# Performance work log

Hardware: AMD Instinct MI355X
Metric: run time of the kernel (lower is better)

The kernel has to match this reference:

```python
import jax, jax.numpy as jnp
import numpy as np

# ---- module hyperparameters (init_kwargs) ----
V0 = 1.0
SIGMA0 = 0.5
GAUSS_CONST = V0 / (np.sqrt(2.0 * np.pi) * SIGMA0)
NW, NF, D, H = 4096, 16, 3, 256  # walkers, fermions, dimensions, hidden width
N = NF * D


def setup_inputs() -> dict:
    key = jax.random.key(0)
    k0, k1, k2, k3 = jax.random.split(key, 4)
    sc = lambda k, shape, fan_in: jax.random.normal(k, shape, jnp.float32) / np.sqrt(fan_in).astype(np.float32)
    return {
        "x": jax.random.normal(k0, (NW, NF, D), jnp.float32),
        "W1": sc(k1, (N, H), N),
        "b1": jnp.zeros((H,), jnp.float32),
        "W2": sc(k2, (H, H), H),
        "b2": jnp.zeros((H,), jnp.float32),
        "w3": sc(k3, (H,), H),
        "b3": jnp.zeros((), jnp.float32),
    }


def _logpsi(xf, W1, b1, W2, b2, w3, b3):
    # xf: (N,) flattened single-walker coordinates -> scalar log|psi|
    h = jnp.tanh(xf @ W1 + b1)
    h = jnp.tanh(h @ W2 + b2)
    return h @ w3 + b3


def reference(x, W1, b1, W2, b2, w3, b3):
    nw, nf, d = x.shape
    xflat = x.reshape(nw, nf * d)

    f = lambda xf: _logpsi(xf, W1, b1, W2, b2, w3, b3)
    grad_f = jax.grad(f)

    def kinetic_one(xf):
        g = grad_f(xf)                      # (N,) d logpsi / dx
        hess = jax.jacfwd(grad_f)(xf)       # (N, N) forward-over-reverse Hessian
        lap = jnp.trace(hess)
        return -0.5 * (lap + jnp.sum(g * g))

    kin = jax.vmap(kinetic_one)(xflat)      # (nw,)

    # harmonic potential 1/2 sum x^2
    pot = 0.5 * jnp.sum(xflat * xflat, axis=1)

    # Gaussian interaction, faithful to source: unsqueeze(-2)/unsqueeze(-1) on
    # (nw, nf, d) broadcasts to (nw, nf, d, d) intra-particle coordinate diffs,
    # then sum over last axis -> (nw, nf, d), triu(k=1) over trailing (nf, d).
    diff = x[..., None, :] - x[..., :, None]            # (nw, nf, d, d)
    sqdist = jnp.sum(diff * diff, axis=-1)              # (nw, nf, d)
    mask = jnp.triu(jnp.ones((nf, d), x.dtype), k=1)    # (nf, d)
    inter = GAUSS_CONST * jnp.sum(jnp.exp(-sqdist / (2.0 * SIGMA0 ** 2)) * mask, axis=(-2, -1))

    eloc = kin + pot + inter
    return (eloc, kin, pot, inter)
```

## Files before the change

### kernel.cpp

```cpp
#include <hip/hip_runtime.h>
#include <cmath>

#define NWALK 4096
#define NXD   48
#define HID   256
#define WPB   8
#define GCONST 0.7978845608028654f

typedef _Float16 half8   __attribute__((ext_vector_type(8)));
typedef float    float4v __attribute__((ext_vector_type(4)));

__global__ __launch_bounds__(256) void prep_all(const float* __restrict__ W2,
                                                const float* __restrict__ W1,
                                                const float* __restrict__ x,
                                                const float* __restrict__ b1,
                                                _Float16* __restrict__ W2c,
                                                _Float16* __restrict__ W1c,
                                                _Float16* __restrict__ t1h,
                                                _Float16* __restrict__ h1h,
                                                _Float16* __restrict__ ch) {
    __shared__ float tile[64][65];
    __shared__ float xs[16][NXD];

    if (blockIdx.x < 16) {
        const int bi = blockIdx.x & 3;
        const int bj = blockIdx.x >> 2;
        const int tx = threadIdx.x & 63;
        const int ty = threadIdx.x >> 6;
        #pragma unroll
        for (int r = 0; r < 16; ++r) {
            int il = ty * 16 + r;
            tile[tx][il] = W2[(bi * 64 + il) * HID + bj * 64 + tx];
        }
        __syncthreads();
        #pragma unroll
        for (int r = 0; r < 16; ++r) {
            int jl = ty * 16 + r;
            W2c[(bj * 64 + jl) * HID + bi * 64 + tx] = (_Float16)tile[jl][tx];
        }
        #pragma unroll
        for (int r = 0; r < 3; ++r) {
            int k = blockIdx.x * 3 + r;
            W1c[k * HID + threadIdx.x] = (_Float16)W1[k * HID + threadIdx.x];
        }
    } else {
        const int i  = threadIdx.x;
        const int w0 = (blockIdx.x - 16) * 16;

        float col[NXD];
        float S = 0.f;
        #pragma unroll
        for (int k = 0; k < NXD; ++k) {
            float v = W1[k * HID + i];
            col[k] = v;
            S = fmaf(v, v, S);
        }
        #pragma unroll
        for (int t = threadIdx.x; t < 16 * NXD; t += 256)
            ((float*)xs)[t] = x[w0 * NXD + t];
        __syncthreads();

        const float b = b1[i];
        #pragma unroll 4
        for (int w = 0; w < 16; ++w) {
            float a1 = b;
            #pragma unroll
            for (int k = 0; k < NXD; ++k)
                a1 = fmaf(xs[w][k], col[k], a1);
            float h1 = tanhf(a1);
            float t1 = 1.f - h1 * h1;
            int off = (w0 + w) * HID + i;
            t1h[off] = (_Float16)t1;
            h1h[off] = (_Float16)h1;
            ch[off]  = (_Float16)(S * h1 * t1);
        }
    }
}

__global__ __launch_bounds__(256, 2) void eloc8(
    const float* __restrict__ x,
    const float* __restrict__ b2,
    const float* __restrict__ w3,
    const _Float16* __restrict__ W2c,
    const _Float16* __restrict__ W1c,
    const _Float16* __restrict__ t1h,
    const _Float16* __restrict__ h1h,
    const _Float16* __restrict__ ch,
    float* __restrict__ out)
{
    __shared__ __align__(16) _Float16 W1s[48 * HID];
    __shared__ float xs[WPB][NXD];
    __shared__ float gw[WPB][4][NXD];
    __shared__ float rt1p[WPB][4][16];
    __shared__ float us[WPB][HID], uhs[WPB][HID];
    __shared__ float b2s[HID], w3s[HID];
    __shared__ float r2s[4][WPB];
    __shared__ float rt2s[WPB];

    const int w0   = blockIdx.x * WPB;
    const int tid  = threadIdx.x;
    const int wave = tid >> 6;
    const int lane = tid & 63;
    const int n16  = lane & 15;
    const int quad = (tid >> 4) & 3;

    half8 afr[8][4];
    #pragma unroll
    for (int s = 0; s < 8; ++s)
        #pragma unroll
        for (int a = 0; a < 4; ++a)
            afr[s][a] = *(const half8*)(W2c + ((wave * 4 + a) * 16 + n16) * HID
                                        + s * 32 + quad * 8);

    b2s[tid] = b2[tid];
    w3s[tid] = w3[tid];
    #pragma unroll
    for (int t = tid; t < WPB * NXD; t += 256)
        ((float*)xs)[t] = x[w0 * NXD + t];

    #pragma unroll
    for (int t = tid; t < 48 * 32; t += 256) {
        int k = t >> 5, c = t & 31;
        half8 wv = *(const half8*)(W1c + k * HID + c * 8);
        *(half8*)(W1s + k * HID + ((c ^ (k & 7)) * 8)) = wv;
    }

    {
        const _Float16* src  = (n16 & 1) ? ch : h1h;
        const _Float16* brow = src + (size_t)(w0 + (n16 >> 1)) * HID;

        float4v acc[4];
        #pragma unroll
        for (int a = 0; a < 4; ++a) acc[a] = (float4v){0.f, 0.f, 0.f, 0.f};
        #pragma unroll
        for (int s = 0; s < 8; ++s) {
            half8 bf = *(const half8*)(brow + (s * 4 + quad) * 8);
            #pragma unroll
            for (int a = 0; a < 4; ++a)
                acc[a] = __builtin_amdgcn_mfma_f32_16x16x32_f16(afr[s][a], bf, acc[a], 0, 0, 0);
        }

        __syncthreads();

        const int w = n16 >> 1;
        float um[4][4];
        #pragma unroll
        for (int a = 0; a < 4; ++a)
            #pragma unroll
            for (int reg = 0; reg < 4; ++reg) um[a][reg] = 0.f;

        if (!(n16 & 1)) {
            #pragma unroll
            for (int a = 0; a < 4; ++a)
                #pragma unroll
                for (int reg = 0; reg < 4; ++reg) {
                    int i    = (wave * 4 + a) * 16 + quad * 4 + reg;
                    float a2 = acc[a][reg] + b2s[i];
                    float h2 = tanhf(a2);
                    float t2 = 1.f - h2 * h2;
                    float u  = w3s[i] * t2;
                    um[a][reg] = u;
                    us [w][i] = u;
                    uhs[w][i] = u * h2;
                }
        }

        float part = 0.f;
        #pragma unroll
        for (int a = 0; a < 4; ++a)
            #pragma unroll
            for (int reg = 0; reg < 4; ++reg) {
                float uo = __shfl_xor(um[a][reg], 1, 64);
                part = fmaf(uo, acc[a][reg], part);
            }
        part += __shfl_xor(part, 16, 64);
        part += __shfl_xor(part, 32, 64);
        if (quad == 0 && (n16 & 1)) r2s[wave][w] = part;
    }
    __syncthreads();
    if (tid < WPB)
        rt2s[tid] = r2s[0][tid] + r2s[1][tid] + r2s[2][tid] + r2s[3][tid];
    __syncthreads();

    #pragma unroll 1
    for (int ww = 0; ww < WPB; ++ww) {
        const int wg = w0 + ww;

        half8 t1f[8];
        #pragma unroll
        for (int s = 0; s < 8; ++s)
            t1f[s] = *(const half8*)(t1h + (size_t)wg * HID + (s * 4 + quad) * 8);

        float4v uu[4];
        #pragma unroll
        for (int a = 0; a < 4; ++a)
            uu[a] = *(const float4v*)(&us[ww][(wave * 4 + a) * 16 + quad * 4]);

        float4v sq[4];
        #pragma unroll
        for (int a = 0; a < 4; ++a) sq[a] = (float4v){0.f, 0.f, 0.f, 0.f};

        #pragma unroll 1
        for (int kt = 0; kt < 3; ++kt) {
            const int krow = kt * 16 + n16;

            half8 w1v[8];
            #pragma unroll
            for (int s = 0; s < 8; ++s)
                w1v[s] = *(const half8*)(W1s + krow * HID
                          + ((((s * 4 + quad) ^ (krow & 7)) << 3)));

            float4v acc[4];
            #pragma unroll
            for (int a = 0; a < 4; ++a) acc[a] = (float4v){0.f, 0.f, 0.f, 0.f};

            __builtin_amdgcn_s_setprio(1);
            #pragma unroll
            for (int s = 0; s < 8; ++s) {
                half8 bf = w1v[s] * t1f[s];
                #pragma unroll
                for (int a = 0; a < 4; ++a)
                    acc[a] = __builtin_amdgcn_mfma_f32_16x16x32_f16(
                        afr[s][a], bf, acc[a], 0, 0, 0);
            }
            __builtin_amdgcn_s_setprio(0);

            float g = 0.f;
            #pragma unroll
            for (int a = 0; a < 4; ++a)
                #pragma unroll
                for (int reg = 0; reg < 4; ++reg) {
                    float m = acc[a][reg];
                    sq[a][reg] = fmaf(m, m, sq[a][reg]);
                    g          = fmaf(m, uu[a][reg], g);
                }
            g += __shfl_xor(g, 16, 64);
            g += __shfl_xor(g, 32, 64);
            if (lane < 16) gw[ww][wave][kt * 16 + lane] = g;
        }

        float rt1 = 0.f;
        #pragma unroll
        for (int a = 0; a < 4; ++a) {
            float4v uh = *(const float4v*)(&uhs[ww][(wave * 4 + a) * 16 + quad * 4]);
            #pragma unroll
            for (int reg = 0; reg < 4; ++reg)
                rt1 = fmaf(sq[a][reg], uh[reg], rt1);
        }
        rt1 += __shfl_xor(rt1, 16, 64);
        rt1 += __shfl_xor(rt1, 32, 64);
        if (lane < 16) rt1p[ww][wave][lane] = rt1;
    }

    __syncthreads();

    const int wa = 2 * wave, wb = wa + 1;
    float rt2a = rt2s[wa];
    float rt2b = rt2s[wb];

    float r0 = rt1p[wa][quad][n16];
    float r1 = rt1p[wb][quad][n16];

    float ga = 0.f, gb = 0.f, xa = 0.f, xb = 0.f;
    if (lane < NXD) {
        ga = gw[wa][0][lane] + gw[wa][1][lane] + gw[wa][2][lane] + gw[wa][3][lane];
        gb = gw[wb][0][lane] + gw[wb][1][lane] + gw[wb][2][lane] + gw[wb][3][lane];
        xa = xs[wa][lane];
        xb = xs[wb][lane];
    }
    float gga = ga * ga, ggb = gb * gb;
    float pa = 0.5f * xa * xa, pb = 0.5f * xb * xb;
    #pragma unroll
    for (int off = 32; off > 0; off >>= 1) {
        r0  += __shfl_down(r0,  off, 64);
        r1  += __shfl_down(r1,  off, 64);
        gga += __shfl_down(gga, off, 64);
        ggb += __shfl_down(ggb, off, 64);
        pa  += __shfl_down(pa,  off, 64);
        pb  += __shfl_down(pb,  off, 64);
    }
    if (lane == 0) {
        float kina = r0 + rt2a - 0.5f * gga;
        float kinb = r1 + rt2b - 0.5f * ggb;

        float x0 = xs[wa][0], x1 = xs[wa][1], x2 = xs[wa][2];
        float x3 = xs[wa][3], x4 = xs[wa][4], x5 = xs[wa][5];
        float d01 = (x0-x1)*(x0-x1) + (x2-x1)*(x2-x1);
        float d02 = (x0-x2)*(x0-x2) + (x1-x2)*(x1-x2);
        float d12 = (x3-x5)*(x3-x5) + (x4-x5)*(x4-x5);
        float intera = GCONST * (expf(-2.f*d01) + expf(-2.f*d02) + expf(-2.f*d12));

        x0 = xs[wb][0]; x1 = xs[wb][1]; x2 = xs[wb][2];
        x3 = xs[wb][3]; x4 = xs[wb][4]; x5 = xs[wb][5];
        float e01 = (x0-x1)*(x0-x1) + (x2-x1)*(x2-x1);
        float e02 = (x0-x2)*(x0-x2) + (x1-x2)*(x1-x2);
        float e12 = (x3-x5)*(x3-x5) + (x4-x5)*(x4-x5);
        float interb = GCONST * (expf(-2.f*e01) + expf(-2.f*e02) + expf(-2.f*e12));

        const int wga = w0 + wa, wgb = w0 + wb;
        out[wga]             = kina + pa + intera;
        out[NWALK + wga]     = kina;
        out[2 * NWALK + wga] = pa;
        out[3 * NWALK + wga] = intera;
        out[wgb]             = kinb + pb + interb;
        out[NWALK + wgb]     = kinb;
        out[2 * NWALK + wgb] = pb;
        out[3 * NWALK + wgb] = interb;
    }
}

extern "C" void kernel_launch(void* const* d_in, const int* in_sizes, int n_in,
                              void* d_out, int out_size, void* d_ws, size_t ws_size,
                              hipStream_t stream) {
    const float* x  = (const float*)d_in[0];
    const float* W1 = (const float*)d_in[1];
    const float* b1 = (const float*)d_in[2];
    const float* W2 = (const float*)d_in[3];
    const float* b2 = (const float*)d_in[4];
    const float* w3 = (const float*)d_in[5];
    float* out = (float*)d_out;

    char* ws = (char*)d_ws;
    _Float16* W2c = (_Float16*)(ws);
    _Float16* W1c = (_Float16*)(ws + 131072);
    _Float16* t1h = (_Float16*)(ws + 155648);
    _Float16* h1h = (_Float16*)(ws + 2252800);
    _Float16* chv = (_Float16*)(ws + 4349952);

    prep_all<<<16 + NWALK / 16, 256, 0, stream>>>(W2, W1, x, b1, W2c, W1c, t1h, h1h, chv);
    eloc8<<<NWALK / WPB, 256, 0, stream>>>(x, b2, w3, W2c, W1c, t1h, h1h, chv, out);
}
```

Measured before the change: 110.3 us.

## Fuse prep kernel into main eloc kernel, computing layer-1 activations in shared memory

Removes the separate prep kernel. Each block now computes its own walkers' layer-1 tanh outputs (t1, h1, and the curvature term) into shared memory, converts W1 to fp16 in the block, and loads W2 transposed straight from fp32 global into MFMA fragments. This drops one kernel launch and the global round trip for the fp16 intermediates. In exchange every block repeats the weight conversion, reads W2 with a strided transposed pattern, and holds 48 W1 column values in registers, which raises register pressure and shared memory use.

```diff
diff --git a/kernel.cpp b/kernel.cpp
--- a/kernel.cpp
+++ b/kernel.cpp
@@ -10,89 +10,23 @@
 typedef _Float16 half8   __attribute__((ext_vector_type(8)));
 typedef float    float4v __attribute__((ext_vector_type(4)));
 
-__global__ __launch_bounds__(256) void prep_all(const float* __restrict__ W2,
-                                                const float* __restrict__ W1,
-                                                const float* __restrict__ x,
-                                                const float* __restrict__ b1,
-                                                _Float16* __restrict__ W2c,
-                                                _Float16* __restrict__ W1c,
-                                                _Float16* __restrict__ t1h,
-                                                _Float16* __restrict__ h1h,
-                                                _Float16* __restrict__ ch) {
-    __shared__ float tile[64][65];
-    __shared__ float xs[16][NXD];
-
-    if (blockIdx.x < 16) {
-        const int bi = blockIdx.x & 3;
-        const int bj = blockIdx.x >> 2;
-        const int tx = threadIdx.x & 63;
-        const int ty = threadIdx.x >> 6;
-        #pragma unroll
-        for (int r = 0; r < 16; ++r) {
-            int il = ty * 16 + r;
-            tile[tx][il] = W2[(bi * 64 + il) * HID + bj * 64 + tx];
-        }
-        __syncthreads();
-        #pragma unroll
-        for (int r = 0; r < 16; ++r) {
-            int jl = ty * 16 + r;
-            W2c[(bj * 64 + jl) * HID + bi * 64 + tx] = (_Float16)tile[jl][tx];
-        }
-        #pragma unroll
-        for (int r = 0; r < 3; ++r) {
-            int k = blockIdx.x * 3 + r;
-            W1c[k * HID + threadIdx.x] = (_Float16)W1[k * HID + threadIdx.x];
-        }
-    } else {
-        const int i  = threadIdx.x;
-        const int w0 = (blockIdx.x - 16) * 16;
-
-        float col[NXD];
-        float S = 0.f;
-        #pragma unroll
-        for (int k = 0; k < NXD; ++k) {
-            float v = W1[k * HID + i];
-            col[k] = v;
-            S = fmaf(v, v, S);
-        }
-        #pragma unroll
-        for (int t = threadIdx.x; t < 16 * NXD; t += 256)
-            ((float*)xs)[t] = x[w0 * NXD + t];
-        __syncthreads();
-
-        const float b = b1[i];
-        #pragma unroll 4
-        for (int w = 0; w < 16; ++w) {
-            float a1 = b;
-            #pragma unroll
-            for (int k = 0; k < NXD; ++k)
-                a1 = fmaf(xs[w][k], col[k], a1);
-            float h1 = tanhf(a1);
-            float t1 = 1.f - h1 * h1;
-            int off = (w0 + w) * HID + i;
-            t1h[off] = (_Float16)t1;
-            h1h[off] = (_Float16)h1;
-            ch[off]  = (_Float16)(S * h1 * t1);
-        }
-    }
-}
-
-__global__ __launch_bounds__(256, 2) void eloc8(
+__global__ __launch_bounds__(256, 2) void eloc_fused(
     const float* __restrict__ x,
+    const float* __restrict__ W1,
+    const float* __restrict__ b1,
+    const float* __restrict__ W2,
     const float* __restrict__ b2,
     const float* __restrict__ w3,
-    const _Float16* __restrict__ W2c,
-    const _Float16* __restrict__ W1c,
-    const _Float16* __restrict__ t1h,
-    const _Float16* __restrict__ h1h,
-    const _Float16* __restrict__ ch,
     float* __restrict__ out)
 {
     __shared__ __align__(16) _Float16 W1s[48 * HID];
+    __shared__ __align__(16) _Float16 t1s[WPB][HID];
+    __shared__ __align__(16) _Float16 h1s[WPB][HID];
+    __shared__ __align__(16) _Float16 chs[WPB][HID];
+    __shared__ float us[WPB][HID], uhs[WPB][HID];
     __shared__ float xs[WPB][NXD];
     __shared__ float gw[WPB][4][NXD];
     __shared__ float rt1p[WPB][4][16];
-    __shared__ float us[WPB][HID], uhs[WPB][HID];
     __shared__ float b2s[HID], w3s[HID];
     __shared__ float r2s[4][WPB];
     __shared__ float rt2s[WPB];
@@ -104,14 +38,6 @@
     const int n16  = lane & 15;
     const int quad = (tid >> 4) & 3;
 
-    half8 afr[8][4];
-    #pragma unroll
-    for (int s = 0; s < 8; ++s)
-        #pragma unroll
-        for (int a = 0; a < 4; ++a)
-            afr[s][a] = *(const half8*)(W2c + ((wave * 4 + a) * 16 + n16) * HID
-                                        + s * 32 + quad * 8);
-
     b2s[tid] = b2[tid];
     w3s[tid] = w3[tid];
     #pragma unroll
@@ -121,13 +47,59 @@
     #pragma unroll
     for (int t = tid; t < 48 * 32; t += 256) {
         int k = t >> 5, c = t & 31;
-        half8 wv = *(const half8*)(W1c + k * HID + c * 8);
-        *(half8*)(W1s + k * HID + ((c ^ (k & 7)) * 8)) = wv;
-    }
+        const float* srcp = W1 + k * HID + c * 8;
+        half8 hv;
+        #pragma unroll
+        for (int e = 0; e < 8; ++e) hv[e] = (_Float16)srcp[e];
+        *(half8*)(W1s + k * HID + ((c ^ (k & 7)) * 8)) = hv;
+    }
+
+    float col[NXD];
+    float S = 0.f;
+    #pragma unroll
+    for (int k = 0; k < NXD; ++k) {
+        float v = W1[k * HID + tid];
+        col[k] = v;
+        S = fmaf(v, v, S);
+    }
+
+    __syncthreads();
 
     {
-        const _Float16* src  = (n16 & 1) ? ch : h1h;
-        const _Float16* brow = src + (size_t)(w0 + (n16 >> 1)) * HID;
+        const float b = b1[tid];
+        #pragma unroll
+        for (int w = 0; w < WPB; ++w) {
+            float a1 = b;
+            #pragma unroll
+            for (int k = 0; k < NXD; ++k)
+                a1 = fmaf(xs[w][k], col[k], a1);
+            float h1 = tanhf(a1);
+            float t1 = 1.f - h1 * h1;
+            t1s[w][tid] = (_Float16)t1;
+            h1s[w][tid] = (_Float16)h1;
+            chs[w][tid] = (_Float16)(S * h1 * t1);
+        }
+    }
+
+    half8 afr[8][4];
+    #pragma unroll
+    for (int s = 0; s < 8; ++s)
+        #pragma unroll
+        for (int a = 0; a < 4; ++a) {
+            const int j  = (wave * 4 + a) * 16 + n16;
+            const int ib = s * 32 + quad * 8;
+            half8 hv;
+            #pragma unroll
+            for (int e = 0; e < 8; ++e)
+                hv[e] = (_Float16)W2[(ib + e) * HID + j];
+            afr[s][a] = hv;
+        }
+
+    __syncthreads();
+
+    {
+        const _Float16* srcb = (n16 & 1) ? &chs[0][0] : &h1s[0][0];
+        const _Float16* brow = srcb + (n16 >> 1) * HID;
 
         float4v acc[4];
         #pragma unroll
@@ -139,8 +111,6 @@
             for (int a = 0; a < 4; ++a)
                 acc[a] = __builtin_amdgcn_mfma_f32_16x16x32_f16(afr[s][a], bf, acc[a], 0, 0, 0);
         }
-
-        __syncthreads();
 
         const int w = n16 >> 1;
         float um[4][4];
@@ -184,12 +154,10 @@
 
     #pragma unroll 1
     for (int ww = 0; ww < WPB; ++ww) {
-        const int wg = w0 + ww;
-
         half8 t1f[8];
         #pragma unroll
         for (int s = 0; s < 8; ++s)
-            t1f[s] = *(const half8*)(t1h + (size_t)wg * HID + (s * 4 + quad) * 8);
+            t1f[s] = *(const half8*)(&t1s[ww][(s * 4 + quad) * 8]);
 
         float4v uu[4];
         #pragma unroll
@@ -320,13 +288,5 @@
     const float* w3 = (const float*)d_in[5];
     float* out = (float*)d_out;
 
-    char* ws = (char*)d_ws;
-    _Float16* W2c = (_Float16*)(ws);
-    _Float16* W1c = (_Float16*)(ws + 131072);
-    _Float16* t1h = (_Float16*)(ws + 155648);
-    _Float16* h1h = (_Float16*)(ws + 2252800);
-    _Float16* chv = (_Float16*)(ws + 4349952);
-
-    prep_all<<<16 + NWALK / 16, 256, 0, stream>>>(W2, W1, x, b1, W2c, W1c, t1h, h1h, chv);
-    eloc8<<<NWALK / WPB, 256, 0, stream>>>(x, b2, w3, W2c, W1c, t1h, h1h, chv, out);
+    eloc_fused<<<NWALK / WPB, 256, 0, stream>>>(x, W1, b1, W2, b2, w3, out);
 }
```

After: 100.3 us (median of 2 runs). 1.1x faster.
